# Kernel tuning notes

Hardware: AMD Instinct MI355X
Metric: run time of the kernel (lower is better)

## Reference

```python
import jax, jax.numpy as jnp
import numpy as np

N_NODES = 100000
N_EDGES = 640000
D_FEAT = 128
UNITS = 128


def setup_inputs() -> dict:
    key = jax.random.key(0)
    k1, k2, k3, k4, k5 = jax.random.split(key, 5)
    X = jax.random.normal(k1, (N_NODES, D_FEAT), dtype=jnp.float32)
    # Glorot-uniform style scaling for the two dense weights
    lim_h = float(np.sqrt(6.0 / (D_FEAT + UNITS)))
    lim_o = float(np.sqrt(6.0 / (UNITS + UNITS)))
    W_hidden = jax.random.uniform(k2, (D_FEAT, UNITS), jnp.float32, -lim_h, lim_h)
    W_out = jax.random.uniform(k3, (UNITS, UNITS), jnp.float32, -lim_o, lim_o)
    b_hidden = jnp.zeros((UNITS,), jnp.float32)
    b_out = jnp.zeros((UNITS,), jnp.float32)
    ref_a = jax.random.randint(k4, (N_EDGES,), 0, N_NODES, dtype=jnp.int32)
    ref_b = jax.random.randint(k5, (N_EDGES,), 0, N_NODES, dtype=jnp.int32)
    return {"X": X, "W_hidden": W_hidden, "b_hidden": b_hidden,
            "W_out": W_out, "b_out": b_out, "ref_a": ref_a, "ref_b": ref_b}


def reference(X, W_hidden, b_hidden, W_out, b_out, ref_a, ref_b):
    # WL1 convolution: X_agg starts as X (self-feature), then undirected
    # scatter-add of neighbor features along both edge directions.
    X_agg = X.at[ref_b].add(X[ref_a])          # a -> b messages
    X_agg = X_agg.at[ref_a].add(X[ref_b])      # b -> a messages (undirected)
    # 2-layer MLP (GIN update) with bias; activation = relu on the output.
    X_hid = X_agg @ W_hidden + b_hidden        # [N, units]
    X_out = X_hid @ W_out + b_out              # [N, units]
    return jax.nn.relu(X_out)
```

## Files before the change

kernel.cpp:

```cpp
#include <hip/hip_runtime.h>
#include <hip/hip_bf16.h>

#define N_NODES 100000
#define N_EDGES 640000
#define D 128
#define NB 98

#define BSZ 64
#define NBKT 1563
#define NBKT_PAD 1568
#define NBLK_AC 64
#define EPB (N_EDGES / NBLK_AC)
#define CAP 3072

typedef unsigned short ushort_t;
typedef __attribute__((ext_vector_type(8))) short short8_t;
typedef __attribute__((ext_vector_type(4))) float floatx4;

static __device__ __forceinline__ ushort_t f32_to_bf16(float f) {
    union { __hip_bfloat16 h; ushort_t u; } c;
    c.h = __float2bfloat16(f);
    return c.u;
}
static __device__ __forceinline__ float bf16_to_f32(ushort_t u) {
    union { unsigned int i; float f; } c;
    c.i = ((unsigned int)u) << 16;
    return c.f;
}

__global__ void combine_weights(const float* __restrict__ Wh,
                                const float* __restrict__ bh,
                                const float* __restrict__ Wo,
                                const float* __restrict__ bo,
                                ushort_t* __restrict__ WcT,
                                float* __restrict__ bc) {
    int gid = blockIdx.x * blockDim.x + threadIdx.x;
    if (gid < D * D) {
        int i = gid >> 7;
        int j = gid & 127;
        float s = 0.f;
        #pragma unroll 4
        for (int k = 0; k < D; ++k)
            s = fmaf(Wh[i * D + k], Wo[k * D + j], s);
        WcT[j * D + i] = f32_to_bf16(s);
    } else if (gid < D * D + D) {
        int j = gid - D * D;
        float s = bo[j];
        #pragma unroll 4
        for (int k = 0; k < D; ++k)
            s = fmaf(bh[k], Wo[k * D + j], s);
        bc[j] = s;
    }
}

__global__ __launch_bounds__(1024)
void hist_k(const int* __restrict__ ra, const int* __restrict__ rb,
            int* __restrict__ hist) {
    __shared__ int h[NBKT_PAD];
    const int t = threadIdx.x;
    for (int i = t; i < NBKT_PAD; i += 1024) h[i] = 0;
    __syncthreads();
    const int base = blockIdx.x * EPB;
    for (int i = t; i < EPB; i += 1024) {
        int a = ra[base + i];
        int b = rb[base + i];
        atomicAdd(&h[a >> 6], 1);
        atomicAdd(&h[b >> 6], 1);
    }
    __syncthreads();
    int* row = hist + blockIdx.x * NBKT_PAD;
    for (int i = t; i < NBKT_PAD; i += 1024) row[i] = h[i];
}

__global__ __launch_bounds__(256)
void scan_hist_k(int* __restrict__ hist, int* __restrict__ btot) {
    const int wave = threadIdx.x >> 6;
    const int lane = threadIdx.x & 63;
    const int bkt = blockIdx.x * 4 + wave;
    if (bkt >= NBKT) return;
    int v = hist[lane * NBKT_PAD + bkt];
    int s = v;
    #pragma unroll
    for (int d = 1; d < 64; d <<= 1) {
        int u = __shfl_up(s, d, 64);
        if (lane >= d) s += u;
    }
    hist[lane * NBKT_PAD + bkt] = s - v;
    if (lane == 63) btot[bkt] = s;
}

__global__ __launch_bounds__(64)
void scan_bkt_k(const int* __restrict__ btot, int* __restrict__ bktbase) {
    const int lane = threadIdx.x;
    int carry = 0;
    for (int c = 0; c < NBKT; c += 64) {
        int idx = c + lane;
        int v = (idx < NBKT) ? btot[idx] : 0;
        int s = v;
        #pragma unroll
        for (int d = 1; d < 64; d <<= 1) {
            int u = __shfl_up(s, d, 64);
            if (lane >= d) s += u;
        }
        if (idx < NBKT) bktbase[idx] = carry + s - v;
        carry += __shfl(s, 63, 64);
    }
}

__global__ __launch_bounds__(1024)
void scatter_k(const int* __restrict__ ra, const int* __restrict__ rb,
               const int* __restrict__ hist, const int* __restrict__ bktbase,
               unsigned* __restrict__ ebuf) {
    __shared__ int cur[NBKT_PAD];
    const int t = threadIdx.x;
    const int* row = hist + blockIdx.x * NBKT_PAD;
    for (int i = t; i < NBKT; i += 1024) cur[i] = bktbase[i] + row[i];
    __syncthreads();
    const int base = blockIdx.x * EPB;
    for (int i = t; i < EPB; i += 1024) {
        int a = ra[base + i];
        int b = rb[base + i];
        int sa = atomicAdd(&cur[a >> 6], 1);
        ebuf[sa] = ((unsigned)(a & 63) << 24) | (unsigned)b;
        int sb = atomicAdd(&cur[b >> 6], 1);
        ebuf[sb] = ((unsigned)(b & 63) << 24) | (unsigned)a;
    }
}

__global__ __launch_bounds__(256)
void resort_k(unsigned* __restrict__ ebuf, const int* __restrict__ bktbase,
              const int* __restrict__ btot, int* __restrict__ off) {
    __shared__ unsigned seg[CAP];
    __shared__ int cnt64[64];
    __shared__ int excl[64];
    const int bkt = blockIdx.x;
    const int t = threadIdx.x;
    const int base = bktbase[bkt];
    int cnt = btot[bkt];
    if (cnt > CAP) cnt = CAP;
    if (t < 64) cnt64[t] = 0;
    __syncthreads();

    for (int i = t; i < cnt; i += 256) {
        unsigned e = ebuf[base + i];
        seg[i] = e;
        atomicAdd(&cnt64[e >> 24], 1);
    }
    __syncthreads();

    if (t < 64) {
        int v = cnt64[t];
        int s = v;
        #pragma unroll
        for (int d = 1; d < 64; d <<= 1) {
            int u = __shfl_up(s, d, 64);
            if (t >= d) s += u;
        }
        excl[t] = s - v;
        cnt64[t] = s - v;
    }
    __syncthreads();

    const int node0 = bkt * BSZ;
    if (t < 64 && node0 + t < N_NODES) off[node0 + t] = base + excl[t];
    if (bkt == NBKT - 1 && t == 0) off[N_NODES] = base + cnt;

    for (int i = t; i < cnt; i += 256) {
        unsigned e = seg[i];
        int pos = atomicAdd(&cnt64[e >> 24], 1);
        ebuf[base + pos] = e & 0xFFFFFF;
    }
}

template<int MODE>
__global__ __launch_bounds__(256)
void gemm_mfma(const float* __restrict__ A, ushort_t* __restrict__ Ybf,
               float* Fout, const ushort_t* __restrict__ WcT,
               const float* __restrict__ bc) {
    __shared__ ushort_t Ws[D][136];
    const int t = threadIdx.x;

    {
        const short8_t* src = (const short8_t*)WcT;
        #pragma unroll
        for (int i = 0; i < 8; ++i) {
            int g = t + i * 256;
            int n = g >> 4;
            int k = (g & 15) * 8;
            *(short8_t*)(&Ws[n][k]) = src[g];
        }
    }
    __syncthreads();

    const int wave = t >> 6;
    const int lane = t & 63;
    const int rowBase = (blockIdx.x * 4 + wave) * 16;
    if (rowBase >= N_NODES) return;

    const int m = rowBase + (lane & 15);
    const int kgrp = lane >> 4;
    const float* arow = (MODE == 0 ? A : (const float*)Fout) + (size_t)m * D;

    short8_t afrag[4];
    #pragma unroll
    for (int kc = 0; kc < 4; ++kc) {
        int k0 = kc * 32 + kgrp * 8;
        float4 lo = *(const float4*)(arow + k0);
        float4 hi = *(const float4*)(arow + k0 + 4);
        short8_t f;
        f[0] = (short)f32_to_bf16(lo.x);
        f[1] = (short)f32_to_bf16(lo.y);
        f[2] = (short)f32_to_bf16(lo.z);
        f[3] = (short)f32_to_bf16(lo.w);
        f[4] = (short)f32_to_bf16(hi.x);
        f[5] = (short)f32_to_bf16(hi.y);
        f[6] = (short)f32_to_bf16(hi.z);
        f[7] = (short)f32_to_bf16(hi.w);
        afrag[kc] = f;
    }

    floatx4 acc[8];
    #pragma unroll
    for (int nt = 0; nt < 8; ++nt)
        acc[nt] = (floatx4){0.f, 0.f, 0.f, 0.f};

    #pragma unroll
    for (int kc = 0; kc < 4; ++kc) {
        const int k0 = kc * 32 + kgrp * 8;
        #pragma unroll
        for (int nt = 0; nt < 8; ++nt) {
            const int n = nt * 16 + (lane & 15);
            short8_t b = *(const short8_t*)(&Ws[n][k0]);
            acc[nt] = __builtin_amdgcn_mfma_f32_16x16x32_bf16(afrag[kc], b, acc[nt], 0, 0, 0);
        }
    }

    const int orow0 = rowBase + (lane >> 4) * 4;
    const int col0 = lane & 15;
    if (MODE == 0) {
        #pragma unroll
        for (int j = 0; j < 4; ++j) {
            size_t base = (size_t)(orow0 + j) * D;
            #pragma unroll
            for (int nt = 0; nt < 8; ++nt)
                Ybf[base + nt * 16 + col0] = f32_to_bf16(acc[nt][j]);
        }
    } else {
        #pragma unroll
        for (int j = 0; j < 4; ++j) {
            size_t base = (size_t)(orow0 + j) * D;
            #pragma unroll
            for (int nt = 0; nt < 8; ++nt) {
                float v = acc[nt][j] + bc[nt * 16 + col0];
                Fout[base + nt * 16 + col0] = fmaxf(v, 0.f);
            }
        }
    }
}

__global__ __launch_bounds__(256)
void gather_bf16(const ushort_t* __restrict__ Y, const int* __restrict__ off,
                 const int* __restrict__ adj, const float* __restrict__ bc,
                 float* __restrict__ out) {
    const int node = blockIdx.x * 8 + (threadIdx.x >> 5);
    const int lane = threadIdx.x & 31;
    float4 acc;
    {
        ushort4 u = *(const ushort4*)(Y + (size_t)node * D + lane * 4);
        acc.x = bf16_to_f32(u.x); acc.y = bf16_to_f32(u.y);
        acc.z = bf16_to_f32(u.z); acc.w = bf16_to_f32(u.w);
    }
    const int s = off[node];
    const int e = off[node + 1];
    int k = s;
    for (; k + 1 < e; k += 2) {
        int n0 = adj[k];
        int n1 = adj[k + 1];
        ushort4 u0 = *(const ushort4*)(Y + (size_t)n0 * D + lane * 4);
        ushort4 u1 = *(const ushort4*)(Y + (size_t)n1 * D + lane * 4);
        acc.x += bf16_to_f32(u0.x); acc.y += bf16_to_f32(u0.y);
        acc.z += bf16_to_f32(u0.z); acc.w += bf16_to_f32(u0.w);
        acc.x += bf16_to_f32(u1.x); acc.y += bf16_to_f32(u1.y);
        acc.z += bf16_to_f32(u1.z); acc.w += bf16_to_f32(u1.w);
    }
    if (k < e) {
        int n0 = adj[k];
        ushort4 u0 = *(const ushort4*)(Y + (size_t)n0 * D + lane * 4);
        acc.x += bf16_to_f32(u0.x); acc.y += bf16_to_f32(u0.y);
        acc.z += bf16_to_f32(u0.z); acc.w += bf16_to_f32(u0.w);
    }
    float4 b = *(const float4*)(bc + lane * 4);
    acc.x = fmaxf(acc.x + b.x, 0.f);
    acc.y = fmaxf(acc.y + b.y, 0.f);
    acc.z = fmaxf(acc.z + b.z, 0.f);
    acc.w = fmaxf(acc.w + b.w, 0.f);
    *(float4*)(out + (size_t)node * D + lane * 4) = acc;
}

__global__ __launch_bounds__(256)
void count_deg(const int* __restrict__ ra, const int* __restrict__ rb,
               int* __restrict__ cnt) {
    int e = blockIdx.x * 256 + threadIdx.x;
    if (e < N_EDGES) {
        atomicAdd(&cnt[ra[e]], 1);
        atomicAdd(&cnt[rb[e]], 1);
    }
}

__global__ __launch_bounds__(256)
void sum_blocks(const int* __restrict__ cnt, int* __restrict__ partials) {
    __shared__ int sm[256];
    int t = threadIdx.x;
    int base = blockIdx.x * 1024 + t * 4;
    int tot = 0;
    #pragma unroll
    for (int i = 0; i < 4; ++i)
        if (base + i < N_NODES) tot += cnt[base + i];
    sm[t] = tot;
    __syncthreads();
    for (int d = 128; d > 0; d >>= 1) {
        if (t < d) sm[t] += sm[t + d];
        __syncthreads();
    }
    if (t == 0) partials[blockIdx.x] = sm[0];
}

__global__ void scan_partials(int* __restrict__ partials, int* __restrict__ off) {
    if (blockIdx.x == 0 && threadIdx.x == 0) {
        int run = 0;
        for (int b = 0; b < NB; ++b) {
            int v = partials[b];
            partials[b] = run;
            run += v;
        }
        off[N_NODES] = run;
    }
}

__global__ __launch_bounds__(256)
void scan_blocks(const int* __restrict__ cnt, const int* __restrict__ partials,
                 int* __restrict__ off, int* __restrict__ cur) {
    __shared__ int sm[256];
    int t = threadIdx.x;
    int base = blockIdx.x * 1024 + t * 4;
    int c[4];
    int tot = 0;
    #pragma unroll
    for (int i = 0; i < 4; ++i) {
        c[i] = (base + i < N_NODES) ? cnt[base + i] : 0;
        tot += c[i];
    }
    sm[t] = tot;
    __syncthreads();
    for (int d = 1; d < 256; d <<= 1) {
        int v = (t >= d) ? sm[t - d] : 0;
        __syncthreads();
        sm[t] += v;
        __syncthreads();
    }
    int excl = sm[t] - tot + partials[blockIdx.x];
    #pragma unroll
    for (int i = 0; i < 4; ++i) {
        int idx = base + i;
        if (idx < N_NODES) {
            off[idx] = excl;
            cur[idx] = excl;
            excl += c[i];
        }
    }
}

__global__ __launch_bounds__(256)
void fill_adj(const int* __restrict__ ra, const int* __restrict__ rb,
              int* __restrict__ cur, int* __restrict__ adj) {
    int e = blockIdx.x * 256 + threadIdx.x;
    if (e < N_EDGES) {
        int a = ra[e];
        int b = rb[e];
        adj[atomicAdd(&cur[a], 1)] = b;
        adj[atomicAdd(&cur[b], 1)] = a;
    }
}

__global__ __launch_bounds__(256)
void gather_f32(const float* __restrict__ Xf, const int* __restrict__ off,
                const int* __restrict__ adj, float* __restrict__ out) {
    const int node = blockIdx.x * 8 + (threadIdx.x >> 5);
    const int lane = threadIdx.x & 31;
    float4 acc = *(const float4*)(Xf + (size_t)node * D + lane * 4);
    const int s = off[node];
    const int e = off[node + 1];
    int k = s;
    for (; k + 1 < e; k += 2) {
        int n0 = adj[k];
        int n1 = adj[k + 1];
        float4 v0 = *(const float4*)(Xf + (size_t)n0 * D + lane * 4);
        float4 v1 = *(const float4*)(Xf + (size_t)n1 * D + lane * 4);
        acc.x += v0.x; acc.y += v0.y; acc.z += v0.z; acc.w += v0.w;
        acc.x += v1.x; acc.y += v1.y; acc.z += v1.z; acc.w += v1.w;
    }
    if (k < e) {
        int n0 = adj[k];
        float4 v0 = *(const float4*)(Xf + (size_t)n0 * D + lane * 4);
        acc.x += v0.x; acc.y += v0.y; acc.z += v0.z; acc.w += v0.w;
    }
    *(float4*)(out + (size_t)node * D + lane * 4) = acc;
}

extern "C" void kernel_launch(void* const* d_in, const int* in_sizes, int n_in,
                              void* d_out, int out_size, void* d_ws, size_t ws_size,
                              hipStream_t stream) {
    const float* X  = (const float*)d_in[0];
    const float* Wh = (const float*)d_in[1];
    const float* bh = (const float*)d_in[2];
    const float* Wo = (const float*)d_in[3];
    const float* bo = (const float*)d_in[4];
    const int* ra   = (const int*)d_in[5];
    const int* rb   = (const int*)d_in[6];
    float* out = (float*)d_out;

    char* p = (char*)d_ws;
    ushort_t* WcT  = (ushort_t*)p; p += (size_t)D * D * 2;
    float* bc      = (float*)p;    p += (size_t)D * 4;
    int* hist      = (int*)p;      p += (size_t)NBLK_AC * NBKT_PAD * 4;
    int* btot      = (int*)p;      p += (size_t)NBKT_PAD * 4;
    int* bktbase   = (int*)p;      p += (size_t)NBKT_PAD * 4;
    int* off       = (int*)p;      p += (size_t)(N_NODES + 4) * 4;
    unsigned* ebuf = (unsigned*)p; p += (size_t)2 * N_EDGES * 4;
    ushort_t* Ybf  = (ushort_t*)p; p += (size_t)N_NODES * D * 2;
    const size_t need = (size_t)(p - (char*)d_ws);
    const bool bigws = ws_size >= need;

    combine_weights<<<(D * D + D + 255) / 256, 256, 0, stream>>>(Wh, bh, Wo, bo, WcT, bc);

    if (bigws) {
        gemm_mfma<0><<<(N_NODES + 63) / 64, 256, 0, stream>>>(X, Ybf, nullptr, WcT, bc);
        hist_k<<<NBLK_AC, 1024, 0, stream>>>(ra, rb, hist);
        scan_hist_k<<<(NBKT + 3) / 4, 256, 0, stream>>>(hist, btot);
        scan_bkt_k<<<1, 64, 0, stream>>>(btot, bktbase);
        scatter_k<<<NBLK_AC, 1024, 0, stream>>>(ra, rb, hist, bktbase, ebuf);
        resort_k<<<NBKT, 256, 0, stream>>>(ebuf, bktbase, btot, off);
        gather_bf16<<<N_NODES / 8, 256, 0, stream>>>(Ybf, off, (const int*)ebuf, bc, out);
    } else {
        char* q = (char*)d_ws;
        ushort_t* WcT2 = (ushort_t*)q; q += (size_t)D * D * 2;
        float* bc2     = (float*)q;    q += (size_t)D * 4;
        int* cnt       = (int*)q;      q += (size_t)N_NODES * 4;
        int* offF      = (int*)q;      q += (size_t)(N_NODES + 4) * 4;
        int* cur       = (int*)q;      q += (size_t)N_NODES * 4;
        int* adj       = (int*)q;      q += (size_t)2 * N_EDGES * 4;
        int* partials  = (int*)q;      q += 448;
        (void)WcT2; (void)bc2;
        hipMemsetAsync(cnt, 0, N_NODES * sizeof(int), stream);
        count_deg<<<N_EDGES / 256, 256, 0, stream>>>(ra, rb, cnt);
        sum_blocks<<<NB, 256, 0, stream>>>(cnt, partials);
        scan_partials<<<1, 64, 0, stream>>>(partials, offF);
        scan_blocks<<<NB, 256, 0, stream>>>(cnt, partials, offF, cur);
        fill_adj<<<N_EDGES / 256, 256, 0, stream>>>(ra, rb, cur, adj);
        gather_f32<<<N_NODES / 8, 256, 0, stream>>>(X, offF, adj, out);
        gemm_mfma<1><<<(N_NODES + 63) / 64, 256, 0, stream>>>(nullptr, nullptr, out, WcT, bc);
    }
}
```

Before: 244.6 us.

## Fuse per-bucket resort into gather using shared-memory neighbor lists

```diff
diff --git a/kernel.cpp b/kernel.cpp
--- a/kernel.cpp
+++ b/kernel.cpp
@@ -127,51 +127,6 @@
     }
 }
 
-__global__ __launch_bounds__(256)
-void resort_k(unsigned* __restrict__ ebuf, const int* __restrict__ bktbase,
-              const int* __restrict__ btot, int* __restrict__ off) {
-    __shared__ unsigned seg[CAP];
-    __shared__ int cnt64[64];
-    __shared__ int excl[64];
-    const int bkt = blockIdx.x;
-    const int t = threadIdx.x;
-    const int base = bktbase[bkt];
-    int cnt = btot[bkt];
-    if (cnt > CAP) cnt = CAP;
-    if (t < 64) cnt64[t] = 0;
-    __syncthreads();
-
-    for (int i = t; i < cnt; i += 256) {
-        unsigned e = ebuf[base + i];
-        seg[i] = e;
-        atomicAdd(&cnt64[e >> 24], 1);
-    }
-    __syncthreads();
-
-    if (t < 64) {
-        int v = cnt64[t];
-        int s = v;
-        #pragma unroll
-        for (int d = 1; d < 64; d <<= 1) {
-            int u = __shfl_up(s, d, 64);
-            if (t >= d) s += u;
-        }
-        excl[t] = s - v;
-        cnt64[t] = s - v;
-    }
-    __syncthreads();
-
-    const int node0 = bkt * BSZ;
-    if (t < 64 && node0 + t < N_NODES) off[node0 + t] = base + excl[t];
-    if (bkt == NBKT - 1 && t == 0) off[N_NODES] = base + cnt;
-
-    for (int i = t; i < cnt; i += 256) {
-        unsigned e = seg[i];
-        int pos = atomicAdd(&cnt64[e >> 24], 1);
-        ebuf[base + pos] = e & 0xFFFFFF;
-    }
-}
-
 template<int MODE>
 __global__ __launch_bounds__(256)
 void gemm_mfma(const float* __restrict__ A, ushort_t* __restrict__ Ybf,
@@ -259,42 +214,91 @@
 }
 
 __global__ __launch_bounds__(256)
-void gather_bf16(const ushort_t* __restrict__ Y, const int* __restrict__ off,
-                 const int* __restrict__ adj, const float* __restrict__ bc,
-                 float* __restrict__ out) {
-    const int node = blockIdx.x * 8 + (threadIdx.x >> 5);
-    const int lane = threadIdx.x & 31;
-    float4 acc;
-    {
-        ushort4 u = *(const ushort4*)(Y + (size_t)node * D + lane * 4);
-        acc.x = bf16_to_f32(u.x); acc.y = bf16_to_f32(u.y);
-        acc.z = bf16_to_f32(u.z); acc.w = bf16_to_f32(u.w);
-    }
-    const int s = off[node];
-    const int e = off[node + 1];
-    int k = s;
-    for (; k + 1 < e; k += 2) {
-        int n0 = adj[k];
-        int n1 = adj[k + 1];
-        ushort4 u0 = *(const ushort4*)(Y + (size_t)n0 * D + lane * 4);
-        ushort4 u1 = *(const ushort4*)(Y + (size_t)n1 * D + lane * 4);
-        acc.x += bf16_to_f32(u0.x); acc.y += bf16_to_f32(u0.y);
-        acc.z += bf16_to_f32(u0.z); acc.w += bf16_to_f32(u0.w);
-        acc.x += bf16_to_f32(u1.x); acc.y += bf16_to_f32(u1.y);
-        acc.z += bf16_to_f32(u1.z); acc.w += bf16_to_f32(u1.w);
-    }
-    if (k < e) {
-        int n0 = adj[k];
-        ushort4 u0 = *(const ushort4*)(Y + (size_t)n0 * D + lane * 4);
-        acc.x += bf16_to_f32(u0.x); acc.y += bf16_to_f32(u0.y);
-        acc.z += bf16_to_f32(u0.z); acc.w += bf16_to_f32(u0.w);
-    }
-    float4 b = *(const float4*)(bc + lane * 4);
-    acc.x = fmaxf(acc.x + b.x, 0.f);
-    acc.y = fmaxf(acc.y + b.y, 0.f);
-    acc.z = fmaxf(acc.z + b.z, 0.f);
-    acc.w = fmaxf(acc.w + b.w, 0.f);
-    *(float4*)(out + (size_t)node * D + lane * 4) = acc;
+void bucket_gather_k(const ushort_t* __restrict__ Ybf,
+                     const unsigned* __restrict__ ebuf,
+                     const int* __restrict__ bktbase,
+                     const int* __restrict__ btot,
+                     const float* __restrict__ bc,
+                     float* __restrict__ out) {
+    __shared__ unsigned seg[CAP];
+    __shared__ unsigned slist[CAP];
+    __shared__ int cnt64[64];
+    __shared__ int start64[64];
+    __shared__ int cur64[64];
+    const int bkt = blockIdx.x;
+    const int t = threadIdx.x;
+    const int base = bktbase[bkt];
+    int cnt = btot[bkt];
+    if (cnt > CAP) cnt = CAP;
+
+    if (t < 64) cnt64[t] = 0;
+    __syncthreads();
+
+    for (int i = t; i < cnt; i += 256) {
+        unsigned e = ebuf[base + i];
+        seg[i] = e;
+        atomicAdd(&cnt64[e >> 24], 1);
+    }
+    __syncthreads();
+
+    if (t < 64) {
+        int v = cnt64[t];
+        int s = v;
+        #pragma unroll
+        for (int d = 1; d < 64; d <<= 1) {
+            int u = __shfl_up(s, d, 64);
+            if (t >= d) s += u;
+        }
+        start64[t] = s - v;
+        cur64[t] = s - v;
+    }
+    __syncthreads();
+
+    for (int i = t; i < cnt; i += 256) {
+        unsigned e = seg[i];
+        int pos = atomicAdd(&cur64[e >> 24], 1);
+        slist[pos] = e & 0xFFFFFFu;
+    }
+    __syncthreads();
+
+    const int g = t >> 5;
+    const int l = t & 31;
+    const int node0 = bkt * BSZ;
+    float4 b4 = *(const float4*)(bc + l * 4);
+    for (int v = g; v < BSZ; v += 8) {
+        const int node = node0 + v;
+        if (node >= N_NODES) break;
+        float4 acc;
+        {
+            ushort4 u = *(const ushort4*)(Ybf + (size_t)node * D + l * 4);
+            acc.x = bf16_to_f32(u.x); acc.y = bf16_to_f32(u.y);
+            acc.z = bf16_to_f32(u.z); acc.w = bf16_to_f32(u.w);
+        }
+        const int s = start64[v];
+        const int e = s + cnt64[v];
+        int k = s;
+        for (; k + 1 < e; k += 2) {
+            int n0 = slist[k];
+            int n1 = slist[k + 1];
+            ushort4 u0 = *(const ushort4*)(Ybf + (size_t)n0 * D + l * 4);
+            ushort4 u1 = *(const ushort4*)(Ybf + (size_t)n1 * D + l * 4);
+            acc.x += bf16_to_f32(u0.x); acc.y += bf16_to_f32(u0.y);
+            acc.z += bf16_to_f32(u0.z); acc.w += bf16_to_f32(u0.w);
+            acc.x += bf16_to_f32(u1.x); acc.y += bf16_to_f32(u1.y);
+            acc.z += bf16_to_f32(u1.z); acc.w += bf16_to_f32(u1.w);
+        }
+        if (k < e) {
+            int n0 = slist[k];
+            ushort4 u0 = *(const ushort4*)(Ybf + (size_t)n0 * D + l * 4);
+            acc.x += bf16_to_f32(u0.x); acc.y += bf16_to_f32(u0.y);
+            acc.z += bf16_to_f32(u0.z); acc.w += bf16_to_f32(u0.w);
+        }
+        acc.x = fmaxf(acc.x + b4.x, 0.f);
+        acc.y = fmaxf(acc.y + b4.y, 0.f);
+        acc.z = fmaxf(acc.z + b4.z, 0.f);
+        acc.w = fmaxf(acc.w + b4.w, 0.f);
+        *(float4*)(out + (size_t)node * D + l * 4) = acc;
+    }
 }
 
 __global__ __launch_bounds__(256)
@@ -425,7 +429,6 @@
     int* hist      = (int*)p;      p += (size_t)NBLK_AC * NBKT_PAD * 4;
     int* btot      = (int*)p;      p += (size_t)NBKT_PAD * 4;
     int* bktbase   = (int*)p;      p += (size_t)NBKT_PAD * 4;
-    int* off       = (int*)p;      p += (size_t)(N_NODES + 4) * 4;
     unsigned* ebuf = (unsigned*)p; p += (size_t)2 * N_EDGES * 4;
     ushort_t* Ybf  = (ushort_t*)p; p += (size_t)N_NODES * D * 2;
     const size_t need = (size_t)(p - (char*)d_ws);
@@ -439,8 +442,7 @@
         scan_hist_k<<<(NBKT + 3) / 4, 256, 0, stream>>>(hist, btot);
         scan_bkt_k<<<1, 64, 0, stream>>>(btot, bktbase);
         scatter_k<<<NBLK_AC, 1024, 0, stream>>>(ra, rb, hist, bktbase, ebuf);
-        resort_k<<<NBKT, 256, 0, stream>>>(ebuf, bktbase, btot, off);
-        gather_bf16<<<N_NODES / 8, 256, 0, stream>>>(Ybf, off, (const int*)ebuf, bc, out);
+        bucket_gather_k<<<NBKT, 256, 0, stream>>>(Ybf, ebuf, bktbase, btot, bc, out);
     } else {
         char* q = (char*)d_ws;
         ushort_t* WcT2 = (ushort_t*)q; q += (size_t)D * D * 2;
```

Result: no change. 242.5 us (-0.9%).
